# Performance work log

Measured on AMD Instinct MI355X. Metric: run time of the kernel, lower is better.

## Reference

```python
import jax, jax.numpy as jnp
import numpy as np

# Assumptions from DCalhas/eeg_to_fmri repo layers:
#  - RandomFourierFeatures: z = cos(x @ W + b) followed by layer normalization
#    over the feature axis (normalization='layer'), W/b trainable.
#  - Sinusoids: elementwise sin(x).

B, D, T, L = 64, 512, 1024, 512

def _layer_norm(x, eps=1e-5):
    mu = jnp.mean(x, axis=-1, keepdims=True)
    var = jnp.var(x, axis=-1, keepdims=True)
    return (x - mu) * jax.lax.rsqrt(var + eps)

def setup_inputs() -> dict:
    key = jax.random.key(0)
    ks = jax.random.split(key, 12)
    s = 1.0 / np.sqrt(L)
    return {
        "x": jax.random.normal(ks[0], (B, D, T), jnp.float32),
        "rff_w": jax.random.normal(ks[1], (D, L), jnp.float32) * (1.0 / np.sqrt(D)),
        "rff_b": jax.random.uniform(ks[2], (L,), jnp.float32, 0.0, 2.0 * np.pi),
        "weight_input": jax.random.normal(ks[3], (L, L), jnp.float32) * s,
        "weight_forget": jax.random.normal(ks[4], (L, L), jnp.float32) * s,
        "weight_context": jax.random.normal(ks[5], (L, L), jnp.float32) * s,
        "recurrent_input": jax.random.normal(ks[6], (L, L), jnp.float32) * s,
        "recurrent_forget": jax.random.normal(ks[7], (L, L), jnp.float32) * s,
        "recurrent_context": jax.random.normal(ks[8], (L, L), jnp.float32) * s,
        "bias_input": jnp.zeros((L,), jnp.float32),
        "bias_forget": jnp.zeros((L,), jnp.float32),
        "bias_context": jnp.zeros((L,), jnp.float32),
        "init_latent": jax.random.normal(ks[9], (1, 1, L), jnp.float32) * s,
        "init_context": jax.random.normal(ks[10], (1, 1, L), jnp.float32) * s,
    }

def reference(x, rff_w, rff_b, weight_input, weight_forget, weight_context,
              recurrent_input, recurrent_forget, recurrent_context,
              bias_input, bias_forget, bias_context, init_latent, init_context):
    b = x.shape[0]
    xt = jnp.transpose(x, (0, 2, 1))                      # [B,T,D]
    z = _layer_norm(jnp.cos(xt @ rff_w + rff_b))          # [B,T,L]
    # hidden_states[t+1] = z_t in the original loop, so the "recurrent" input
    # at step t is z_{t-1} (init_latent at t=0). Gates are thus batchable.
    z_prev = jnp.concatenate(
        [jnp.broadcast_to(init_latent, (b, 1, z.shape[2])), z[:, :-1]], axis=1)
    i = jax.nn.sigmoid(z @ weight_input + z_prev @ recurrent_input + bias_input)
    f = jax.nn.sigmoid(z @ weight_forget + z_prev @ recurrent_forget + bias_forget)
    g = jnp.tanh(z @ weight_context + z_prev @ recurrent_context + bias_context)
    o = jnp.sin(z)                                        # Sinusoids gate

    c0 = jnp.broadcast_to(init_context[:, 0], (b, z.shape[2]))  # [B,L]
    def step(c_prev, gates):
        i_t, f_t, g_t, o_t = gates
        c_t = f_t * c_prev + i_t * g_t
        return c_t, o_t * c_t
    xs = tuple(jnp.transpose(a, (1, 0, 2)) for a in (i, f, g, o))  # time-major
    _, h = jax.lax.scan(step, c0, xs)                     # [T,B,L]
    return jnp.transpose(h, (1, 2, 0))                    # [B,L,T]
```

## Files before the change

### kernel.cpp

```cpp
#include <hip/hip_runtime.h>
#include <hip/hip_bf16.h>
#include <hip/hip_fp16.h>
#include <cstdint>
#include <cstddef>


typedef float f32x4 __attribute__((ext_vector_type(4)));
typedef short s16x8 __attribute__((ext_vector_type(8)));

__device__ __forceinline__ void gload_lds16(const void* g, void* l) {
  __builtin_amdgcn_global_load_lds(
      (const __attribute__((address_space(1))) void*)g,
      (__attribute__((address_space(3))) void*)l, 16, 0, 0);
}
__device__ __forceinline__ ushort f2bf(float f) {
  uint32_t u = __float_as_uint(f);
  return (ushort)((u + 0x7FFF + ((u >> 16) & 1)) >> 16);
}
__device__ __forceinline__ float bf2f(ushort s) {
  return __uint_as_float(((uint32_t)s) << 16);
}
__device__ __forceinline__ ushort f2h(float f) {
  return __half_as_ushort(__float2half(f));
}
__device__ __forceinline__ float h2f(ushort s) {
  return __half2float(__ushort_as_half(s));
}

#define MF(d, a, b) d = __builtin_amdgcn_mfma_f32_16x16x32_bf16(a, b, d, 0, 0, 0);

__global__ __launch_bounds__(256) void transpose8(
    const float* __restrict__ s0, const float* __restrict__ s1,
    const float* __restrict__ s2, const float* __restrict__ s3,
    const float* __restrict__ s4, const float* __restrict__ s5,
    const float* __restrict__ il, const float* __restrict__ W1,
    ushort* __restrict__ W2t, ushort* __restrict__ ilb,
    ushort* __restrict__ W1t)
{
  const int z = blockIdx.z;
  if (z == 6) {
    if (blockIdx.x == 0 && blockIdx.y == 0) {
      ilb[threadIdx.x] = f2bf(il[threadIdx.x]);
      ilb[threadIdx.x + 256] = f2bf(il[threadIdx.x + 256]);
    }
    return;
  }
  const float* src = z == 0 ? s0 : z == 1 ? s1 : z == 2 ? s2
                   : z == 3 ? s3 : z == 4 ? s4 : z == 5 ? s5 : W1;
  ushort* dst = (z == 7) ? W1t
              : W2t + (size_t)(z >> 1) * 512 * 1024 + (z & 1) * 512;
  const int ld = (z == 7) ? 512 : 1024;
  __shared__ float tile[32][33];
  const int c0 = blockIdx.x * 32, r0 = blockIdx.y * 32;
  const int tx = threadIdx.x & 31, ty = threadIdx.x >> 5;
#pragma unroll
  for (int i = 0; i < 4; ++i)
    tile[ty + i * 8][tx] = src[(size_t)(r0 + ty + i * 8) * 512 + c0 + tx];
  __syncthreads();
#pragma unroll
  for (int i = 0; i < 4; ++i)
    dst[(size_t)(c0 + ty + i * 8) * ld + r0 + tx] = f2bf(tile[tx][ty + i * 8]);
}

__global__ __launch_bounds__(256) void transpose_x(
    const float* __restrict__ x, ushort* __restrict__ xt)
{
  __shared__ float tile[64][68];
  const int b = blockIdx.z;
  const int t0 = blockIdx.x * 64, d0 = blockIdx.y * 64;
  const float* src = x + ((size_t)b * 512 + d0) * 1024 + t0;
  const int lr_ = threadIdx.x >> 4, lc4 = (threadIdx.x & 15) * 4;
#pragma unroll
  for (int p = 0; p < 4; ++p) {
    const float4 v = *(const float4*)(src + (size_t)(lr_ + p * 16) * 1024 + lc4);
    *(float4*)&tile[lr_ + p * 16][lc4] = v;
  }
  __syncthreads();
  const int tt = threadIdx.x >> 2, dc = (threadIdx.x & 3) * 16;
  ushort* dst = xt + ((size_t)b * 1024 + t0 + tt) * 512 + d0 + dc;
  uint4 o1, o2;
  o1.x = (uint)f2bf(tile[dc + 0][tt]) | ((uint)f2bf(tile[dc + 1][tt]) << 16);
  o1.y = (uint)f2bf(tile[dc + 2][tt]) | ((uint)f2bf(tile[dc + 3][tt]) << 16);
  o1.z = (uint)f2bf(tile[dc + 4][tt]) | ((uint)f2bf(tile[dc + 5][tt]) << 16);
  o1.w = (uint)f2bf(tile[dc + 6][tt]) | ((uint)f2bf(tile[dc + 7][tt]) << 16);
  o2.x = (uint)f2bf(tile[dc + 8][tt]) | ((uint)f2bf(tile[dc + 9][tt]) << 16);
  o2.y = (uint)f2bf(tile[dc + 10][tt]) | ((uint)f2bf(tile[dc + 11][tt]) << 16);
  o2.z = (uint)f2bf(tile[dc + 12][tt]) | ((uint)f2bf(tile[dc + 13][tt]) << 16);
  o2.w = (uint)f2bf(tile[dc + 14][tt]) | ((uint)f2bf(tile[dc + 15][tt]) << 16);
  *(uint4*)(dst) = o1;
  *(uint4*)(dst + 8) = o2;
}

__global__ __launch_bounds__(256, 2) void k1_mfma(
    const ushort* __restrict__ A, const ushort* __restrict__ Bt,
    const float* __restrict__ bias, ushort* __restrict__ U)
{
  __shared__ __align__(16) short As[128 * 64];
  __shared__ __align__(16) short Bs[128 * 64];
  const int tid = threadIdx.x;
  const int lane = tid & 63, wid = tid >> 6;
  const int orig = blockIdx.x;
  const int swz = (orig & 7) * 256 + (orig >> 3);
  const int n0 = (swz & 3) * 128, r0 = (swz >> 2) * 128;
  const int wr = wid >> 1, wc = wid & 1;
  const int fr = lane & 15, fq = lane >> 4;
  const int lr = lane >> 3;
  const int swz_el = ((lane & 7) ^ lr) * 8;

  const int RA = r0 + wid * 32 + lr;
  const ushort* pa0 = A + (size_t)(RA)      * 512 + swz_el;
  const ushort* pa1 = A + (size_t)(RA + 8)  * 512 + swz_el;
  const ushort* pa2 = A + (size_t)(RA + 16) * 512 + swz_el;
  const ushort* pa3 = A + (size_t)(RA + 24) * 512 + swz_el;
  const int RB = n0 + wid * 32 + lr;
  const ushort* pb0 = Bt + (size_t)(RB)      * 512 + swz_el;
  const ushort* pb1 = Bt + (size_t)(RB + 8)  * 512 + swz_el;
  const ushort* pb2 = Bt + (size_t)(RB + 16) * 512 + swz_el;
  const ushort* pb3 = Bt + (size_t)(RB + 24) * 512 + swz_el;
  char* dA = (char*)As + wid * 4096;
  char* dB = (char*)Bs + wid * 4096;

  const int so0 = fr * 64 + ((fq)     ^ (fr & 7)) * 8;
  const int so1 = fr * 64 + ((4 + fq) ^ (fr & 7)) * 8;

  f32x4 c00 = {0.f,0.f,0.f,0.f}, c01 = c00, c02 = c00, c03 = c00,
        c10 = c00, c11 = c00, c12 = c00, c13 = c00,
        c20 = c00, c21 = c00, c22 = c00, c23 = c00,
        c30 = c00, c31 = c00, c32 = c00, c33 = c00;

  for (int k0 = 0; k0 < 512; k0 += 64) {
    gload_lds16(pa0 + k0, dA);        gload_lds16(pa1 + k0, dA + 1024);
    gload_lds16(pa2 + k0, dA + 2048); gload_lds16(pa3 + k0, dA + 3072);
    gload_lds16(pb0 + k0, dB);        gload_lds16(pb1 + k0, dB + 1024);
    gload_lds16(pb2 + k0, dB + 2048); gload_lds16(pb3 + k0, dB + 3072);
    __syncthreads();
    const s16x8 a00 = *(const s16x8*)&As[wr * 4096 + 0 * 1024 + so0];
    const s16x8 a01 = *(const s16x8*)&As[wr * 4096 + 0 * 1024 + so1];
    const s16x8 a10 = *(const s16x8*)&As[wr * 4096 + 1 * 1024 + so0];
    const s16x8 a11 = *(const s16x8*)&As[wr * 4096 + 1 * 1024 + so1];
    const s16x8 a20 = *(const s16x8*)&As[wr * 4096 + 2 * 1024 + so0];
    const s16x8 a21 = *(const s16x8*)&As[wr * 4096 + 2 * 1024 + so1];
    const s16x8 a30 = *(const s16x8*)&As[wr * 4096 + 3 * 1024 + so0];
    const s16x8 a31 = *(const s16x8*)&As[wr * 4096 + 3 * 1024 + so1];
    const s16x8 b00 = *(const s16x8*)&Bs[wc * 4096 + 0 * 1024 + so0];
    const s16x8 b01 = *(const s16x8*)&Bs[wc * 4096 + 0 * 1024 + so1];
    const s16x8 b10 = *(const s16x8*)&Bs[wc * 4096 + 1 * 1024 + so0];
    const s16x8 b11 = *(const s16x8*)&Bs[wc * 4096 + 1 * 1024 + so1];
    const s16x8 b20 = *(const s16x8*)&Bs[wc * 4096 + 2 * 1024 + so0];
    const s16x8 b21 = *(const s16x8*)&Bs[wc * 4096 + 2 * 1024 + so1];
    const s16x8 b30 = *(const s16x8*)&Bs[wc * 4096 + 3 * 1024 + so0];
    const s16x8 b31 = *(const s16x8*)&Bs[wc * 4096 + 3 * 1024 + so1];
    MF(c00, a00, b00) MF(c01, a00, b10) MF(c02, a00, b20) MF(c03, a00, b30)
    MF(c10, a10, b00) MF(c11, a10, b10) MF(c12, a10, b20) MF(c13, a10, b30)
    MF(c20, a20, b00) MF(c21, a20, b10) MF(c22, a20, b20) MF(c23, a20, b30)
    MF(c30, a30, b00) MF(c31, a30, b10) MF(c32, a30, b20) MF(c33, a30, b30)
    MF(c00, a01, b01) MF(c01, a01, b11) MF(c02, a01, b21) MF(c03, a01, b31)
    MF(c10, a11, b01) MF(c11, a11, b11) MF(c12, a11, b21) MF(c13, a11, b31)
    MF(c20, a21, b01) MF(c21, a21, b11) MF(c22, a21, b21) MF(c23, a21, b31)
    MF(c30, a31, b01) MF(c31, a31, b11) MF(c32, a31, b21) MF(c33, a31, b31)
    __syncthreads();
  }

#define EPI1(cmn, m_, n_) { \
    const int col = n0 + wc * 64 + n_ * 16 + fr; \
    const float bv = bias[col]; \
    const int rbase = r0 + wr * 64 + m_ * 16 + fq * 4; \
    _Pragma("unroll") for (int j = 0; j < 4; ++j) \
      U[(size_t)(rbase + j) * 512 + col] = f2bf(cosf(cmn[j] + bv)); }
  EPI1(c00, 0, 0) EPI1(c01, 0, 1) EPI1(c02, 0, 2) EPI1(c03, 0, 3)
  EPI1(c10, 1, 0) EPI1(c11, 1, 1) EPI1(c12, 1, 2) EPI1(c13, 1, 3)
  EPI1(c20, 2, 0) EPI1(c21, 2, 1) EPI1(c22, 2, 2) EPI1(c23, 2, 3)
  EPI1(c30, 3, 0) EPI1(c31, 3, 1) EPI1(c32, 3, 2) EPI1(c33, 3, 3)
#undef EPI1
}

__global__ __launch_bounds__(256) void ln_rows(
    const ushort* __restrict__ U, ushort* __restrict__ Z)
{
  const int row = blockIdx.x * 4 + (threadIdx.x >> 6);
  const int lane = threadIdx.x & 63;
  const size_t base = (size_t)row * 512 + lane * 8;
  const uint4 pk = *(const uint4*)(U + base);
  float v[8];
  v[0] = bf2f(pk.x & 0xffff); v[1] = bf2f(pk.x >> 16);
  v[2] = bf2f(pk.y & 0xffff); v[3] = bf2f(pk.y >> 16);
  v[4] = bf2f(pk.z & 0xffff); v[5] = bf2f(pk.z >> 16);
  v[6] = bf2f(pk.w & 0xffff); v[7] = bf2f(pk.w >> 16);
  float s = 0.f, s2 = 0.f;
#pragma unroll
  for (int j = 0; j < 8; ++j) { s += v[j]; s2 += v[j] * v[j]; }
#pragma unroll
  for (int m = 1; m < 64; m <<= 1) { s += __shfl_xor(s, m); s2 += __shfl_xor(s2, m); }
  const float mean = s * (1.f / 512.f);
  const float var = s2 * (1.f / 512.f) - mean * mean;
  const float inv = rsqrtf(var + 1e-5f);
  uint4 o;
  o.x = (uint)f2bf((v[0] - mean) * inv) | ((uint)f2bf((v[1] - mean) * inv) << 16);
  o.y = (uint)f2bf((v[2] - mean) * inv) | ((uint)f2bf((v[3] - mean) * inv) << 16);
  o.z = (uint)f2bf((v[4] - mean) * inv) | ((uint)f2bf((v[5] - mean) * inv) << 16);
  o.w = (uint)f2bf((v[6] - mean) * inv) | ((uint)f2bf((v[7] - mean) * inv) << 16);
  *(uint4*)(Z + base) = o;
}

__global__ __launch_bounds__(256, 2) void k2_mfma(
    const ushort* __restrict__ Z, const ushort* __restrict__ Wt,
    const ushort* __restrict__ IL,
    const float* __restrict__ biv, const float* __restrict__ bfv,
    const float* __restrict__ bcv,
    ushort* __restrict__ G2, int tc, int Tc, int nwg)
{
  __shared__ __align__(16) short As[128 * 64];
  __shared__ __align__(16) short Bs0[128 * 64];
  __shared__ __align__(16) short Bs1[128 * 64];
  const int tid = threadIdx.x;
  const int lane = tid & 63, wid = tid >> 6;
  const int cpx = nwg >> 3;
  const int orig = blockIdx.x;
  const int swz = (orig & 7) * cpx + (orig >> 3);
  const int bx = swz % 6, by = swz / 6;
  const int nb = Tc >> 7;
  const int b = by / nb, tb = by % nb;
  const int r0g = b * 1024 + tc + tb * 128;
  const int r0c = b * Tc + tb * 128;
  const bool isig = bx < 4;
  const int n0 = isig ? bx * 128 : 0;
  const int fb = bx - 4;
  const int wr = wid >> 1, wc = wid & 1;
  const int fr = lane & 15, fq = lane >> 4;
  const int lr = lane >> 3;
  const int swz_el = ((lane & 7) ^ lr) * 8;

  const int R0 = r0g + wid * 32 + lr;
  const ushort* pa0 = Z + (size_t)(R0)      * 512 + swz_el;
  const ushort* pa1 = Z + (size_t)(R0 + 8)  * 512 + swz_el;
  const ushort* pa2 = Z + (size_t)(R0 + 16) * 512 + swz_el;
  const ushort* pa3 = Z + (size_t)(R0 + 24) * 512 + swz_el;
  const ushort* ph0 = ((((R0)      & 1023) == 0) ? IL : (Z + (size_t)(R0 - 1)  * 512)) + swz_el;
  const ushort* ph1 = ((((R0 + 8)  & 1023) == 0) ? IL : (Z + (size_t)(R0 + 7)  * 512)) + swz_el;
  const ushort* ph2 = ((((R0 + 16) & 1023) == 0) ? IL : (Z + (size_t)(R0 + 15) * 512)) + swz_el;
  const ushort* ph3 = ((((R0 + 24) & 1023) == 0) ? IL : (Z + (size_t)(R0 + 23) * 512)) + swz_el;
  const int RB0 = (isig ? n0 : 512 + fb * 256) + wid * 32 + lr;
  const ushort* pb0 = Wt + (size_t)(RB0)      * 1024 + swz_el;
  const ushort* pb1 = Wt + (size_t)(RB0 + 8)  * 1024 + swz_el;
  const ushort* pb2 = Wt + (size_t)(RB0 + 16) * 1024 + swz_el;
  const ushort* pb3 = Wt + (size_t)(RB0 + 24) * 1024 + swz_el;
  const int RB1 = (isig ? 1024 + n0 : 512 + fb * 256 + 128) + wid * 32 + lr;
  const ushort* pq0 = Wt + (size_t)(RB1)      * 1024 + swz_el;
  const ushort* pq1 = Wt + (size_t)(RB1 + 8)  * 1024 + swz_el;
  const ushort* pq2 = Wt + (size_t)(RB1 + 16) * 1024 + swz_el;
  const ushort* pq3 = Wt + (size_t)(RB1 + 24) * 1024 + swz_el;

  const int so0 = fr * 64 + ((fq)     ^ (fr & 7)) * 8;
  const int so1 = fr * 64 + ((4 + fq) ^ (fr & 7)) * 8;

  f32x4 zz = {0.f,0.f,0.f,0.f};
  f32x4 c00=zz,c01=zz,c02=zz,c03=zz, c10=zz,c11=zz,c12=zz,c13=zz,
        c20=zz,c21=zz,c22=zz,c23=zz, c30=zz,c31=zz,c32=zz,c33=zz;
  f32x4 d00=zz,d01=zz,d02=zz,d03=zz, d10=zz,d11=zz,d12=zz,d13=zz,
        d20=zz,d21=zz,d22=zz,d23=zz, d30=zz,d31=zz,d32=zz,d33=zz;

#define STG8(P0,P1,P2,P3, KO, DST) { \
    char* d_ = (char*)(DST) + wid * 4096; \
    gload_lds16((P0) + (KO), d_);        gload_lds16((P1) + (KO), d_ + 1024); \
    gload_lds16((P2) + (KO), d_ + 2048); gload_lds16((P3) + (KO), d_ + 3072); }

#define RDA(SO) \
    const s16x8 fa0 = *(const s16x8*)&As[wr * 4096 + 0 * 1024 + (SO)]; \
    const s16x8 fa1 = *(const s16x8*)&As[wr * 4096 + 1 * 1024 + (SO)]; \
    const s16x8 fa2 = *(const s16x8*)&As[wr * 4096 + 2 * 1024 + (SO)]; \
    const s16x8 fa3 = *(const s16x8*)&As[wr * 4096 + 3 * 1024 + (SO)];

#define RDB(BS, SO) \
    const s16x8 fb0 = *(const s16x8*)&(BS)[wc * 4096 + 0 * 1024 + (SO)]; \
    const s16x8 fb1 = *(const s16x8*)&(BS)[wc * 4096 + 1 * 1024 + (SO)]; \
    const s16x8 fb2 = *(const s16x8*)&(BS)[wc * 4096 + 2 * 1024 + (SO)]; \
    const s16x8 fb3 = *(const s16x8*)&(BS)[wc * 4096 + 3 * 1024 + (SO)];

#define MMC \
    MF(c00,fa0,fb0) MF(c01,fa0,fb1) MF(c02,fa0,fb2) MF(c03,fa0,fb3) \
    MF(c10,fa1,fb0) MF(c11,fa1,fb1) MF(c12,fa1,fb2) MF(c13,fa1,fb3) \
    MF(c20,fa2,fb0) MF(c21,fa2,fb1) MF(c22,fa2,fb2) MF(c23,fa2,fb3) \
    MF(c30,fa3,fb0) MF(c31,fa3,fb1) MF(c32,fa3,fb2) MF(c33,fa3,fb3)

#define MMD \
    MF(d00,fa0,fb0) MF(d01,fa0,fb1) MF(d02,fa0,fb2) MF(d03,fa0,fb3) \
    MF(d10,fa1,fb0) MF(d11,fa1,fb1) MF(d12,fa1,fb2) MF(d13,fa1,fb3) \
    MF(d20,fa2,fb0) MF(d21,fa2,fb1) MF(d22,fa2,fb2) MF(d23,fa2,fb3) \
    MF(d30,fa3,fb0) MF(d31,fa3,fb1) MF(d32,fa3,fb2) MF(d33,fa3,fb3)

#define KSTEP(SO_) { \
    RDA(SO_) \
    { RDB(Bs0, SO_) MMC } \
    { RDB(Bs1, SO_) MMD } }

  for (int k0 = 0; k0 < 512; k0 += 64) {
    STG8(pa0, pa1, pa2, pa3, k0, As)
    STG8(pb0, pb1, pb2, pb3, k0, Bs0)
    STG8(pq0, pq1, pq2, pq3, k0, Bs1)
    __syncthreads();
    KSTEP(so0)
    KSTEP(so1)
    __syncthreads();
  }
  for (int k0 = 0; k0 < 512; k0 += 64) {
    STG8(ph0, ph1, ph2, ph3, k0, As)
    STG8(pb0, pb1, pb2, pb3, 512 + k0, Bs0)
    STG8(pq0, pq1, pq2, pq3, 512 + k0, Bs1)
    __syncthreads();
    KSTEP(so0)
    KSTEP(so1)
    __syncthreads();
  }
#undef KSTEP
#undef MMD
#undef MMC
#undef RDB
#undef RDA
#undef STG8

  if (isig) {
#define EPI(cmn, dmn, m_, n_) { \
    const int col = n0 + wc * 64 + n_ * 16 + fr; \
    const float bvi = biv[col], bvc = bcv[col]; \
    const int rbase = wr * 64 + m_ * 16 + fq * 4; \
    _Pragma("unroll") for (int j = 0; j < 4; ++j) { \
      const float iv = 1.f / (1.f + __expf(-(cmn[j] + bvi))); \
      const float gv = 2.f / (1.f + __expf(-2.f * (dmn[j] + bvc))) - 1.f; \
      G2[(size_t)(r0c + rbase + j) * 1024 + col] = f2h(iv * gv); } }
    EPI(c00, d00, 0, 0) EPI(c01, d01, 0, 1) EPI(c02, d02, 0, 2) EPI(c03, d03, 0, 3)
    EPI(c10, d10, 1, 0) EPI(c11, d11, 1, 1) EPI(c12, d12, 1, 2) EPI(c13, d13, 1, 3)
    EPI(c20, d20, 2, 0) EPI(c21, d21, 2, 1) EPI(c22, d22, 2, 2) EPI(c23, d23, 2, 3)
    EPI(c30, d30, 3, 0) EPI(c31, d31, 3, 1) EPI(c32, d32, 3, 2) EPI(c33, d33, 3, 3)
#undef EPI
  } else {
#define EPIF(cmn, m_, n_, COFF) { \
    const int col = fb * 256 + (COFF) + wc * 64 + n_ * 16 + fr; \
    const float bv = bfv[col]; \
    const int rbase = wr * 64 + m_ * 16 + fq * 4; \
    _Pragma("unroll") for (int j = 0; j < 4; ++j) { \
      const float fv = 1.f / (1.f + __expf(-(cmn[j] + bv))); \
      G2[(size_t)(r0c + rbase + j) * 1024 + 512 + col] = f2h(fv); } }
    EPIF(c00, 0, 0, 0) EPIF(c01, 0, 1, 0) EPIF(c02, 0, 2, 0) EPIF(c03, 0, 3, 0)
    EPIF(c10, 1, 0, 0) EPIF(c11, 1, 1, 0) EPIF(c12, 1, 2, 0) EPIF(c13, 1, 3, 0)
    EPIF(c20, 2, 0, 0) EPIF(c21, 2, 1, 0) EPIF(c22, 2, 2, 0) EPIF(c23, 2, 3, 0)
    EPIF(c30, 3, 0, 0) EPIF(c31, 3, 1, 0) EPIF(c32, 3, 2, 0) EPIF(c33, 3, 3, 0)
    EPIF(d00, 0, 0, 128) EPIF(d01, 0, 1, 128) EPIF(d02, 0, 2, 128) EPIF(d03, 0, 3, 128)
    EPIF(d10, 1, 0, 128) EPIF(d11, 1, 1, 128) EPIF(d12, 1, 2, 128) EPIF(d13, 1, 3, 128)
    EPIF(d20, 2, 0, 128) EPIF(d21, 2, 1, 128) EPIF(d22, 2, 2, 128) EPIF(d23, 2, 3, 128)
    EPIF(d30, 3, 0, 128) EPIF(d31, 3, 1, 128) EPIF(d32, 3, 2, 128) EPIF(d33, 3, 3, 128)
#undef EPIF
  }
}

__global__ __launch_bounds__(256) void k3a_seg(
    const ushort* __restrict__ G2, float* __restrict__ Aseg,
    float* __restrict__ Bseg, int Tc)
{
  const int l = blockIdx.x * 256 + threadIdx.x;
  const int b = blockIdx.y, s = blockIdx.z;
  const int SEGc = Tc >> 6;
  const ushort* gb = G2 + ((size_t)(b * Tc + s * 64)) * 1024 + l;
  float A = 1.f, c = 0.f;
#pragma unroll 8
  for (int j = 0; j < 64; ++j) {
    const float P = h2f(gb[(size_t)j * 1024]);
    const float F = h2f(gb[(size_t)j * 1024 + 512]);
    A *= F;
    c = fmaf(F, c, P);
  }
  const size_t o = (size_t)(b * SEGc + s) * 512 + l;
  Aseg[o] = A;
  Bseg[o] = c;
}

__global__ __launch_bounds__(512) void k3b_comb(
    const float* __restrict__ Aseg, const float* __restrict__ Bseg,
    const float* __restrict__ initc, float* __restrict__ cstart,
    float* __restrict__ cbuf, int tc, int Tc)
{
  const int b = blockIdx.x, l = threadIdx.x;
  const int SEGc = Tc >> 6;
  float c = (tc == 0) ? initc[l] : cbuf[b * 512 + l];
  for (int s = 0; s < SEGc; ++s) {
    const size_t o = (size_t)(b * SEGc + s) * 512 + l;
    cstart[o] = c;
    c = fmaf(Aseg[o], c, Bseg[o]);
  }
  cbuf[b * 512 + l] = c;
}

__global__ __launch_bounds__(128) void k3c_emit(
    const ushort* __restrict__ G2, const ushort* __restrict__ Z,
    const float* __restrict__ cstart, float* __restrict__ out,
    int tc, int Tc)
{
  __shared__ float tile[128][65];
  const int tid = threadIdx.x;
  const int l0 = blockIdx.x * 128;
  const int b = blockIdx.y, s = blockIdx.z;
  const int SEGc = Tc >> 6;
  const int l = l0 + tid;

  float c = cstart[(size_t)(b * SEGc + s) * 512 + l];
  const ushort* gb = G2 + ((size_t)(b * Tc + s * 64)) * 1024 + l;
  const ushort* zb = Z + ((size_t)(b * 1024 + tc + s * 64)) * 512 + l;
#pragma unroll 8
  for (int j = 0; j < 64; ++j) {
    const float P = h2f(gb[(size_t)j * 1024]);
    const float F = h2f(gb[(size_t)j * 1024 + 512]);
    const float zv = bf2f(zb[(size_t)j * 512]);
    c = fmaf(F, c, P);
    tile[tid][j] = sinf(zv) * c;
  }
  __syncthreads();
  const int col = tid & 63, rhalf = tid >> 6;
  const size_t obase = ((size_t)b * 512 + l0) * 1024 + (size_t)(tc + s * 64) + col;
#pragma unroll
  for (int p = 0; p < 64; ++p) {
    const int row = rhalf + p * 2;
    out[obase + (size_t)row * 1024] = tile[row][col];
  }
}

extern "C" void kernel_launch(void* const* d_in, const int* in_sizes, int n_in,
                              void* d_out, int out_size, void* d_ws, size_t ws_size,
                              hipStream_t stream)
{
  const float* x  = (const float*)d_in[0];
  const float* W  = (const float*)d_in[1];
  const float* rb = (const float*)d_in[2];
  const float* wi = (const float*)d_in[3];
  const float* wf = (const float*)d_in[4];
  const float* wc = (const float*)d_in[5];
  const float* ri = (const float*)d_in[6];
  const float* rf = (const float*)d_in[7];
  const float* rc = (const float*)d_in[8];
  const float* bi = (const float*)d_in[9];
  const float* bfo = (const float*)d_in[10];
  const float* bc = (const float*)d_in[11];
  const float* il = (const float*)d_in[12];
  const float* ic = (const float*)d_in[13];
  float* out = (float*)d_out;

  char* ws = (char*)d_ws;
  size_t off = 0;
  auto alloc = [&](size_t bytes) -> void* {
    void* p = ws + off;
    off = (off + bytes + 255) & ~(size_t)255;
    return p;
  };
  ushort* z    = (ushort*)alloc((size_t)65536 * 512 * 2);
  ushort* W1t  = (ushort*)alloc((size_t)512 * 512 * 2);
  ushort* W2t  = (ushort*)alloc((size_t)1536 * 1024 * 2);
  ushort* ilb  = (ushort*)alloc(512 * 2);
  float*  cbuf = (float*)alloc((size_t)64 * 512 * 4);
  float*  Aseg = (float*)alloc((size_t)64 * 16 * 512 * 4);
  float*  Bseg = (float*)alloc((size_t)64 * 16 * 512 * 4);
  float*  cstart = (float*)alloc((size_t)64 * 16 * 512 * 4);
  const size_t fixed_end = off;
  ushort* xt   = (ushort*)alloc((size_t)65536 * 512 * 2);
  ushort* G2   = (ushort*)(ws + fixed_end);
  ushort* u    = (ushort*)d_out;

  int Tc = 1024;
  while (Tc > 128 && fixed_end + (size_t)64 * Tc * 1024 * 2 > ws_size) Tc >>= 1;

  transpose8<<<dim3(16, 16, 8), 256, 0, stream>>>(
      wi, ri, wf, rf, wc, rc, il, W, W2t, ilb, W1t);
  transpose_x<<<dim3(16, 8, 64), 256, 0, stream>>>(x, xt);

  k1_mfma<<<dim3(2048), 256, 0, stream>>>(xt, W1t, rb, u);
  ln_rows<<<16384, 256, 0, stream>>>(u, z);

  for (int tc = 0; tc < 1024; tc += Tc) {
    const int SEGc = Tc >> 6;
    const int nwg2 = 6 * 64 * (Tc >> 7);
    k2_mfma<<<dim3(nwg2), 256, 0, stream>>>(
        z, W2t, ilb, bi, bfo, bc, G2, tc, Tc, nwg2);
    k3a_seg<<<dim3(2, 64, SEGc), 256, 0, stream>>>(G2, Aseg, Bseg, Tc);
    k3b_comb<<<64, 512, 0, stream>>>(Aseg, Bseg, ic, cstart, cbuf, tc, Tc);
    k3c_emit<<<dim3(4, 64, SEGc), 128, 0, stream>>>(G2, z, cstart, out, tc, Tc);
  }
}
```

Before: 534.9 us.

## Fuse layer norm into RFF GEMM epilogue with full-row 64x512 tiles

The first GEMM now computes whole 64-row by 512-column output tiles per block, so cos and the layer-norm statistics can be computed in the epilogue using shuffle and shared-memory reductions. The normalized bf16 result is written directly to z. This removes the separate ln_rows kernel and the bf16 round trip through an intermediate buffer. In exchange LDS use grows (the whole 512x64 B slice is staged each k-step), there are 32 accumulator tiles per wave, and the grid is halved, which may cut occupancy.

After: 636.6 us. 19.0% more time.

```diff
diff --git a/kernel.cpp b/kernel.cpp
--- a/kernel.cpp
+++ b/kernel.cpp
@@ -93,113 +93,127 @@
 
 __global__ __launch_bounds__(256, 2) void k1_mfma(
     const ushort* __restrict__ A, const ushort* __restrict__ Bt,
-    const float* __restrict__ bias, ushort* __restrict__ U)
-{
-  __shared__ __align__(16) short As[128 * 64];
-  __shared__ __align__(16) short Bs[128 * 64];
+    const float* __restrict__ bias, ushort* __restrict__ Z)
+{
+  __shared__ __align__(16) short As[64 * 64];
+  __shared__ __align__(16) short Bs[512 * 64];
+  __shared__ float redS[4][64], redS2[4][64], redM[64], redI[64];
   const int tid = threadIdx.x;
   const int lane = tid & 63, wid = tid >> 6;
   const int orig = blockIdx.x;
-  const int swz = (orig & 7) * 256 + (orig >> 3);
-  const int n0 = (swz & 3) * 128, r0 = (swz >> 2) * 128;
-  const int wr = wid >> 1, wc = wid & 1;
+  const int swz = (orig & 7) * 128 + (orig >> 3);
+  const int r0 = swz * 64;
   const int fr = lane & 15, fq = lane >> 4;
   const int lr = lane >> 3;
   const int swz_el = ((lane & 7) ^ lr) * 8;
 
-  const int RA = r0 + wid * 32 + lr;
-  const ushort* pa0 = A + (size_t)(RA)      * 512 + swz_el;
-  const ushort* pa1 = A + (size_t)(RA + 8)  * 512 + swz_el;
-  const ushort* pa2 = A + (size_t)(RA + 16) * 512 + swz_el;
-  const ushort* pa3 = A + (size_t)(RA + 24) * 512 + swz_el;
-  const int RB = n0 + wid * 32 + lr;
-  const ushort* pb0 = Bt + (size_t)(RB)      * 512 + swz_el;
-  const ushort* pb1 = Bt + (size_t)(RB + 8)  * 512 + swz_el;
-  const ushort* pb2 = Bt + (size_t)(RB + 16) * 512 + swz_el;
-  const ushort* pb3 = Bt + (size_t)(RB + 24) * 512 + swz_el;
-  char* dA = (char*)As + wid * 4096;
-  char* dB = (char*)Bs + wid * 4096;
-
-  const int so0 = fr * 64 + ((fq)     ^ (fr & 7)) * 8;
-  const int so1 = fr * 64 + ((4 + fq) ^ (fr & 7)) * 8;
-
-  f32x4 c00 = {0.f,0.f,0.f,0.f}, c01 = c00, c02 = c00, c03 = c00,
-        c10 = c00, c11 = c00, c12 = c00, c13 = c00,
-        c20 = c00, c21 = c00, c22 = c00, c23 = c00,
-        c30 = c00, c31 = c00, c32 = c00, c33 = c00;
+  const int RA = r0 + wid * 16 + lr;
+  const ushort* pa0 = A + (size_t)(RA)     * 512 + swz_el;
+  const ushort* pa1 = A + (size_t)(RA + 8) * 512 + swz_el;
+  const ushort* pb = Bt + (size_t)(wid * 128 + lr) * 512 + swz_el;
+  char* dA = (char*)As + wid * 2048;
+  char* dB = (char*)Bs + wid * 16384;
+
+  const int so0 = ((fq)     ^ (fr & 7)) * 8;
+  const int so1 = ((4 + fq) ^ (fr & 7)) * 8;
+
+  f32x4 zz = {0.f,0.f,0.f,0.f};
+  f32x4 c00=zz,c01=zz,c02=zz,c03=zz,c04=zz,c05=zz,c06=zz,c07=zz,
+        c10=zz,c11=zz,c12=zz,c13=zz,c14=zz,c15=zz,c16=zz,c17=zz,
+        c20=zz,c21=zz,c22=zz,c23=zz,c24=zz,c25=zz,c26=zz,c27=zz,
+        c30=zz,c31=zz,c32=zz,c33=zz,c34=zz,c35=zz,c36=zz,c37=zz;
+
+#define KS(SO_) { \
+    const s16x8 fa0 = *(const s16x8*)&As[(0 * 16 + fr) * 64 + (SO_)]; \
+    const s16x8 fa1 = *(const s16x8*)&As[(1 * 16 + fr) * 64 + (SO_)]; \
+    const s16x8 fa2 = *(const s16x8*)&As[(2 * 16 + fr) * 64 + (SO_)]; \
+    const s16x8 fa3 = *(const s16x8*)&As[(3 * 16 + fr) * 64 + (SO_)]; \
+    const s16x8 fb0 = *(const s16x8*)&Bs[(wid * 128 + 0 * 16 + fr) * 64 + (SO_)]; \
+    const s16x8 fb1 = *(const s16x8*)&Bs[(wid * 128 + 1 * 16 + fr) * 64 + (SO_)]; \
+    const s16x8 fb2 = *(const s16x8*)&Bs[(wid * 128 + 2 * 16 + fr) * 64 + (SO_)]; \
+    const s16x8 fb3 = *(const s16x8*)&Bs[(wid * 128 + 3 * 16 + fr) * 64 + (SO_)]; \
+    const s16x8 fb4 = *(const s16x8*)&Bs[(wid * 128 + 4 * 16 + fr) * 64 + (SO_)]; \
+    const s16x8 fb5 = *(const s16x8*)&Bs[(wid * 128 + 5 * 16 + fr) * 64 + (SO_)]; \
+    const s16x8 fb6 = *(const s16x8*)&Bs[(wid * 128 + 6 * 16 + fr) * 64 + (SO_)]; \
+    const s16x8 fb7 = *(const s16x8*)&Bs[(wid * 128 + 7 * 16 + fr) * 64 + (SO_)]; \
+    MF(c00,fa0,fb0) MF(c01,fa0,fb1) MF(c02,fa0,fb2) MF(c03,fa0,fb3) \
+    MF(c04,fa0,fb4) MF(c05,fa0,fb5) MF(c06,fa0,fb6) MF(c07,fa0,fb7) \
+    MF(c10,fa1,fb0) MF(c11,fa1,fb1) MF(c12,fa1,fb2) MF(c13,fa1,fb3) \
+    MF(c14,fa1,fb4) MF(c15,fa1,fb5) MF(c16,fa1,fb6) MF(c17,fa1,fb7) \
+    MF(c20,fa2,fb0) MF(c21,fa2,fb1) MF(c22,fa2,fb2) MF(c23,fa2,fb3) \
+    MF(c24,fa2,fb4) MF(c25,fa2,fb5) MF(c26,fa2,fb6) MF(c27,fa2,fb7) \
+    MF(c30,fa3,fb0) MF(c31,fa3,fb1) MF(c32,fa3,fb2) MF(c33,fa3,fb3) \
+    MF(c34,fa3,fb4) MF(c35,fa3,fb5) MF(c36,fa3,fb6) MF(c37,fa3,fb7) }
 
   for (int k0 = 0; k0 < 512; k0 += 64) {
-    gload_lds16(pa0 + k0, dA);        gload_lds16(pa1 + k0, dA + 1024);
-    gload_lds16(pa2 + k0, dA + 2048); gload_lds16(pa3 + k0, dA + 3072);
-    gload_lds16(pb0 + k0, dB);        gload_lds16(pb1 + k0, dB + 1024);
-    gload_lds16(pb2 + k0, dB + 2048); gload_lds16(pb3 + k0, dB + 3072);
-    __syncthreads();
-    const s16x8 a00 = *(const s16x8*)&As[wr * 4096 + 0 * 1024 + so0];
-    const s16x8 a01 = *(const s16x8*)&As[wr * 4096 + 0 * 1024 + so1];
-    const s16x8 a10 = *(const s16x8*)&As[wr * 4096 + 1 * 1024 + so0];
-    const s16x8 a11 = *(const s16x8*)&As[wr * 4096 + 1 * 1024 + so1];
-    const s16x8 a20 = *(const s16x8*)&As[wr * 4096 + 2 * 1024 + so0];
-    const s16x8 a21 = *(const s16x8*)&As[wr * 4096 + 2 * 1024 + so1];
-    const s16x8 a30 = *(const s16x8*)&As[wr * 4096 + 3 * 1024 + so0];
-    const s16x8 a31 = *(const s16x8*)&As[wr * 4096 + 3 * 1024 + so1];
-    const s16x8 b00 = *(const s16x8*)&Bs[wc * 4096 + 0 * 1024 + so0];
-    const s16x8 b01 = *(const s16x8*)&Bs[wc * 4096 + 0 * 1024 + so1];
-    const s16x8 b10 = *(const s16x8*)&Bs[wc * 4096 + 1 * 1024 + so0];
-    const s16x8 b11 = *(const s16x8*)&Bs[wc * 4096 + 1 * 1024 + so1];
-    const s16x8 b20 = *(const s16x8*)&Bs[wc * 4096 + 2 * 1024 + so0];
-    const s16x8 b21 = *(const s16x8*)&Bs[wc * 4096 + 2 * 1024 + so1];
-    const s16x8 b30 = *(const s16x8*)&Bs[wc * 4096 + 3 * 1024 + so0];
-    const s16x8 b31 = *(const s16x8*)&Bs[wc * 4096 + 3 * 1024 + so1];
-    MF(c00, a00, b00) MF(c01, a00, b10) MF(c02, a00, b20) MF(c03, a00, b30)
-    MF(c10, a10, b00) MF(c11, a10, b10) MF(c12, a10, b20) MF(c13, a10, b30)
-    MF(c20, a20, b00) MF(c21, a20, b10) MF(c22, a20, b20) MF(c23, a20, b30)
-    MF(c30, a30, b00) MF(c31, a30, b10) MF(c32, a30, b20) MF(c33, a30, b30)
-    MF(c00, a01, b01) MF(c01, a01, b11) MF(c02, a01, b21) MF(c03, a01, b31)
-    MF(c10, a11, b01) MF(c11, a11, b11) MF(c12, a11, b21) MF(c13, a11, b31)
-    MF(c20, a21, b01) MF(c21, a21, b11) MF(c22, a21, b21) MF(c23, a21, b31)
-    MF(c30, a31, b01) MF(c31, a31, b11) MF(c32, a31, b21) MF(c33, a31, b31)
-    __syncthreads();
-  }
-
-#define EPI1(cmn, m_, n_) { \
-    const int col = n0 + wc * 64 + n_ * 16 + fr; \
-    const float bv = bias[col]; \
-    const int rbase = r0 + wr * 64 + m_ * 16 + fq * 4; \
-    _Pragma("unroll") for (int j = 0; j < 4; ++j) \
-      U[(size_t)(rbase + j) * 512 + col] = f2bf(cosf(cmn[j] + bv)); }
-  EPI1(c00, 0, 0) EPI1(c01, 0, 1) EPI1(c02, 0, 2) EPI1(c03, 0, 3)
-  EPI1(c10, 1, 0) EPI1(c11, 1, 1) EPI1(c12, 1, 2) EPI1(c13, 1, 3)
-  EPI1(c20, 2, 0) EPI1(c21, 2, 1) EPI1(c22, 2, 2) EPI1(c23, 2, 3)
-  EPI1(c30, 3, 0) EPI1(c31, 3, 1) EPI1(c32, 3, 2) EPI1(c33, 3, 3)
-#undef EPI1
-}
-
-__global__ __launch_bounds__(256) void ln_rows(
-    const ushort* __restrict__ U, ushort* __restrict__ Z)
-{
-  const int row = blockIdx.x * 4 + (threadIdx.x >> 6);
-  const int lane = threadIdx.x & 63;
-  const size_t base = (size_t)row * 512 + lane * 8;
-  const uint4 pk = *(const uint4*)(U + base);
-  float v[8];
-  v[0] = bf2f(pk.x & 0xffff); v[1] = bf2f(pk.x >> 16);
-  v[2] = bf2f(pk.y & 0xffff); v[3] = bf2f(pk.y >> 16);
-  v[4] = bf2f(pk.z & 0xffff); v[5] = bf2f(pk.z >> 16);
-  v[6] = bf2f(pk.w & 0xffff); v[7] = bf2f(pk.w >> 16);
-  float s = 0.f, s2 = 0.f;
+    gload_lds16(pa0 + k0, dA);
+    gload_lds16(pa1 + k0, dA + 1024);
 #pragma unroll
-  for (int j = 0; j < 8; ++j) { s += v[j]; s2 += v[j] * v[j]; }
-#pragma unroll
-  for (int m = 1; m < 64; m <<= 1) { s += __shfl_xor(s, m); s2 += __shfl_xor(s2, m); }
-  const float mean = s * (1.f / 512.f);
-  const float var = s2 * (1.f / 512.f) - mean * mean;
-  const float inv = rsqrtf(var + 1e-5f);
-  uint4 o;
-  o.x = (uint)f2bf((v[0] - mean) * inv) | ((uint)f2bf((v[1] - mean) * inv) << 16);
-  o.y = (uint)f2bf((v[2] - mean) * inv) | ((uint)f2bf((v[3] - mean) * inv) << 16);
-  o.z = (uint)f2bf((v[4] - mean) * inv) | ((uint)f2bf((v[5] - mean) * inv) << 16);
-  o.w = (uint)f2bf((v[6] - mean) * inv) | ((uint)f2bf((v[7] - mean) * inv) << 16);
-  *(uint4*)(Z + base) = o;
+    for (int g = 0; g < 16; ++g)
+      gload_lds16(pb + (size_t)g * 8 * 512 + k0, dB + g * 1024);
+    __syncthreads();
+    KS(so0)
+    KS(so1)
+    __syncthreads();
+  }
+#undef KS
+
+  f32x4 ps0 = zz, ps1 = zz, ps2 = zz, ps3 = zz;
+  f32x4 pq0 = zz, pq1 = zz, pq2 = zz, pq3 = zz;
+#define CB(d, mm, n_) { \
+    const float bv = bias[wid * 128 + n_ * 16 + fr]; \
+    f32x4 t; \
+    _Pragma("unroll") for (int j = 0; j < 4; ++j) t[j] = cosf(d[j] + bv); \
+    d = t; ps##mm += t; pq##mm += t * t; }
+  CB(c00,0,0) CB(c01,0,1) CB(c02,0,2) CB(c03,0,3)
+  CB(c04,0,4) CB(c05,0,5) CB(c06,0,6) CB(c07,0,7)
+  CB(c10,1,0) CB(c11,1,1) CB(c12,1,2) CB(c13,1,3)
+  CB(c14,1,4) CB(c15,1,5) CB(c16,1,6) CB(c17,1,7)
+  CB(c20,2,0) CB(c21,2,1) CB(c22,2,2) CB(c23,2,3)
+  CB(c24,2,4) CB(c25,2,5) CB(c26,2,6) CB(c27,2,7)
+  CB(c30,3,0) CB(c31,3,1) CB(c32,3,2) CB(c33,3,3)
+  CB(c34,3,4) CB(c35,3,5) CB(c36,3,6) CB(c37,3,7)
+#undef CB
+
+#define RED2(PS, PQ, m_) \
+  _Pragma("unroll") for (int j = 0; j < 4; ++j) { \
+    float s = PS[j], s2 = PQ[j]; \
+    _Pragma("unroll") for (int msk = 1; msk < 16; msk <<= 1) { \
+      s += __shfl_xor(s, msk); s2 += __shfl_xor(s2, msk); } \
+    if (fr == 0) { \
+      redS[wid][m_ * 16 + fq * 4 + j] = s; \
+      redS2[wid][m_ * 16 + fq * 4 + j] = s2; } }
+  RED2(ps0, pq0, 0)
+  RED2(ps1, pq1, 1)
+  RED2(ps2, pq2, 2)
+  RED2(ps3, pq3, 3)
+#undef RED2
+  __syncthreads();
+  if (tid < 64) {
+    const float s  = redS[0][tid] + redS[1][tid] + redS[2][tid] + redS[3][tid];
+    const float s2 = redS2[0][tid] + redS2[1][tid] + redS2[2][tid] + redS2[3][tid];
+    const float mean = s * (1.f / 512.f);
+    const float var = s2 * (1.f / 512.f) - mean * mean;
+    redM[tid] = mean;
+    redI[tid] = rsqrtf(var + 1e-5f);
+  }
+  __syncthreads();
+
+  ushort* Zp = Z + (size_t)r0 * 512;
+#define ZW(d, m_, n_) { \
+    _Pragma("unroll") for (int j = 0; j < 4; ++j) { \
+      const int row = m_ * 16 + fq * 4 + j; \
+      Zp[(size_t)row * 512 + wid * 128 + n_ * 16 + fr] = \
+          f2bf((d[j] - redM[row]) * redI[row]); } }
+  ZW(c00,0,0) ZW(c01,0,1) ZW(c02,0,2) ZW(c03,0,3)
+  ZW(c04,0,4) ZW(c05,0,5) ZW(c06,0,6) ZW(c07,0,7)
+  ZW(c10,1,0) ZW(c11,1,1) ZW(c12,1,2) ZW(c13,1,3)
+  ZW(c14,1,4) ZW(c15,1,5) ZW(c16,1,6) ZW(c17,1,7)
+  ZW(c20,2,0) ZW(c21,2,1) ZW(c22,2,2) ZW(c23,2,3)
+  ZW(c24,2,4) ZW(c25,2,5) ZW(c26,2,6) ZW(c27,2,7)
+  ZW(c30,3,0) ZW(c31,3,1) ZW(c32,3,2) ZW(c33,3,3)
+  ZW(c34,3,4) ZW(c35,3,5) ZW(c36,3,6) ZW(c37,3,7)
+#undef ZW
 }
 
 __global__ __launch_bounds__(256, 2) void k2_mfma(
@@ -460,7 +474,6 @@
   const size_t fixed_end = off;
   ushort* xt   = (ushort*)alloc((size_t)65536 * 512 * 2);
   ushort* G2   = (ushort*)(ws + fixed_end);
-  ushort* u    = (ushort*)d_out;
 
   int Tc = 1024;
   while (Tc > 128 && fixed_end + (size_t)64 * Tc * 1024 * 2 > ws_size) Tc >>= 1;
@@ -469,8 +482,7 @@
       wi, ri, wf, rf, wc, rc, il, W, W2t, ilb, W1t);
   transpose_x<<<dim3(16, 8, 64), 256, 0, stream>>>(x, xt);
 
-  k1_mfma<<<dim3(2048), 256, 0, stream>>>(xt, W1t, rb, u);
-  ln_rows<<<16384, 256, 0, stream>>>(u, z);
+  k1_mfma<<<dim3(1024), 256, 0, stream>>>(xt, W1t, rb, z);
 
   for (int tc = 0; tc < 1024; tc += Tc) {
     const int SEGc = Tc >> 6;
```

## Merge prep transposes and fold segment combine into emit kernel

Applied to the files above, without the earlier changes.

Combines the weight transpose and x transpose into one launch, removes the serial k3b combine kernel by having each emit block recompute its segment start carry from the per-segment A/B values, and vectorises the segment scan to two lanes per thread with packed loads. The goal is fewer kernel launches and dropping the cstart buffer round-trip. In exchange there is redundant prefix work in every emit block, and the prep launch now includes many early-exit blocks. The recompute loop is hardcoded to 15 segments and stays correct only while SEGc is at most 16.

New measurement: 532.9 us. Within noise of the previous version (-0.4%).

```diff
diff --git a/kernel.cpp b/kernel.cpp
--- a/kernel.cpp
+++ b/kernel.cpp
@@ -29,15 +29,44 @@
 
 #define MF(d, a, b) d = __builtin_amdgcn_mfma_f32_16x16x32_bf16(a, b, d, 0, 0, 0);
 
-__global__ __launch_bounds__(256) void transpose8(
+__global__ __launch_bounds__(256) void prep_all(
     const float* __restrict__ s0, const float* __restrict__ s1,
     const float* __restrict__ s2, const float* __restrict__ s3,
     const float* __restrict__ s4, const float* __restrict__ s5,
     const float* __restrict__ il, const float* __restrict__ W1,
+    const float* __restrict__ x,
     ushort* __restrict__ W2t, ushort* __restrict__ ilb,
-    ushort* __restrict__ W1t)
-{
+    ushort* __restrict__ W1t, ushort* __restrict__ xt)
+{
+  __shared__ float tile[64][68];
   const int z = blockIdx.z;
+  if (z >= 8) {
+    if (blockIdx.y >= 8) return;
+    const int b = z - 8;
+    const int t0 = blockIdx.x * 64, d0 = blockIdx.y * 64;
+    const float* src = x + ((size_t)b * 512 + d0) * 1024 + t0;
+    const int lr_ = threadIdx.x >> 4, lc4 = (threadIdx.x & 15) * 4;
+#pragma unroll
+    for (int p = 0; p < 4; ++p) {
+      const float4 v = *(const float4*)(src + (size_t)(lr_ + p * 16) * 1024 + lc4);
+      *(float4*)&tile[lr_ + p * 16][lc4] = v;
+    }
+    __syncthreads();
+    const int tt = threadIdx.x >> 2, dc = (threadIdx.x & 3) * 16;
+    ushort* dst = xt + ((size_t)b * 1024 + t0 + tt) * 512 + d0 + dc;
+    uint4 o1, o2;
+    o1.x = (uint)f2bf(tile[dc + 0][tt]) | ((uint)f2bf(tile[dc + 1][tt]) << 16);
+    o1.y = (uint)f2bf(tile[dc + 2][tt]) | ((uint)f2bf(tile[dc + 3][tt]) << 16);
+    o1.z = (uint)f2bf(tile[dc + 4][tt]) | ((uint)f2bf(tile[dc + 5][tt]) << 16);
+    o1.w = (uint)f2bf(tile[dc + 6][tt]) | ((uint)f2bf(tile[dc + 7][tt]) << 16);
+    o2.x = (uint)f2bf(tile[dc + 8][tt]) | ((uint)f2bf(tile[dc + 9][tt]) << 16);
+    o2.y = (uint)f2bf(tile[dc + 10][tt]) | ((uint)f2bf(tile[dc + 11][tt]) << 16);
+    o2.z = (uint)f2bf(tile[dc + 12][tt]) | ((uint)f2bf(tile[dc + 13][tt]) << 16);
+    o2.w = (uint)f2bf(tile[dc + 14][tt]) | ((uint)f2bf(tile[dc + 15][tt]) << 16);
+    *(uint4*)(dst) = o1;
+    *(uint4*)(dst + 8) = o2;
+    return;
+  }
   if (z == 6) {
     if (blockIdx.x == 0 && blockIdx.y == 0) {
       ilb[threadIdx.x] = f2bf(il[threadIdx.x]);
@@ -50,45 +79,16 @@
   ushort* dst = (z == 7) ? W1t
               : W2t + (size_t)(z >> 1) * 512 * 1024 + (z & 1) * 512;
   const int ld = (z == 7) ? 512 : 1024;
-  __shared__ float tile[32][33];
+  float (*t32)[33] = (float(*)[33])&tile[0][0];
   const int c0 = blockIdx.x * 32, r0 = blockIdx.y * 32;
   const int tx = threadIdx.x & 31, ty = threadIdx.x >> 5;
 #pragma unroll
   for (int i = 0; i < 4; ++i)
-    tile[ty + i * 8][tx] = src[(size_t)(r0 + ty + i * 8) * 512 + c0 + tx];
+    t32[ty + i * 8][tx] = src[(size_t)(r0 + ty + i * 8) * 512 + c0 + tx];
   __syncthreads();
 #pragma unroll
   for (int i = 0; i < 4; ++i)
-    dst[(size_t)(c0 + ty + i * 8) * ld + r0 + tx] = f2bf(tile[tx][ty + i * 8]);
-}
-
-__global__ __launch_bounds__(256) void transpose_x(
-    const float* __restrict__ x, ushort* __restrict__ xt)
-{
-  __shared__ float tile[64][68];
-  const int b = blockIdx.z;
-  const int t0 = blockIdx.x * 64, d0 = blockIdx.y * 64;
-  const float* src = x + ((size_t)b * 512 + d0) * 1024 + t0;
-  const int lr_ = threadIdx.x >> 4, lc4 = (threadIdx.x & 15) * 4;
-#pragma unroll
-  for (int p = 0; p < 4; ++p) {
-    const float4 v = *(const float4*)(src + (size_t)(lr_ + p * 16) * 1024 + lc4);
-    *(float4*)&tile[lr_ + p * 16][lc4] = v;
-  }
-  __syncthreads();
-  const int tt = threadIdx.x >> 2, dc = (threadIdx.x & 3) * 16;
-  ushort* dst = xt + ((size_t)b * 1024 + t0 + tt) * 512 + d0 + dc;
-  uint4 o1, o2;
-  o1.x = (uint)f2bf(tile[dc + 0][tt]) | ((uint)f2bf(tile[dc + 1][tt]) << 16);
-  o1.y = (uint)f2bf(tile[dc + 2][tt]) | ((uint)f2bf(tile[dc + 3][tt]) << 16);
-  o1.z = (uint)f2bf(tile[dc + 4][tt]) | ((uint)f2bf(tile[dc + 5][tt]) << 16);
-  o1.w = (uint)f2bf(tile[dc + 6][tt]) | ((uint)f2bf(tile[dc + 7][tt]) << 16);
-  o2.x = (uint)f2bf(tile[dc + 8][tt]) | ((uint)f2bf(tile[dc + 9][tt]) << 16);
-  o2.y = (uint)f2bf(tile[dc + 10][tt]) | ((uint)f2bf(tile[dc + 11][tt]) << 16);
-  o2.z = (uint)f2bf(tile[dc + 12][tt]) | ((uint)f2bf(tile[dc + 13][tt]) << 16);
-  o2.w = (uint)f2bf(tile[dc + 14][tt]) | ((uint)f2bf(tile[dc + 15][tt]) << 16);
-  *(uint4*)(dst) = o1;
-  *(uint4*)(dst + 8) = o2;
+    dst[(size_t)(c0 + ty + i * 8) * ld + r0 + tx] = f2bf(t32[tx][ty + i * 8]);
 }
 
 __global__ __launch_bounds__(256, 2) void k1_mfma(
@@ -356,43 +356,32 @@
     const ushort* __restrict__ G2, float* __restrict__ Aseg,
     float* __restrict__ Bseg, int Tc)
 {
-  const int l = blockIdx.x * 256 + threadIdx.x;
-  const int b = blockIdx.y, s = blockIdx.z;
+  const int l2 = threadIdx.x * 2;
+  const int b = blockIdx.x, s = blockIdx.y;
   const int SEGc = Tc >> 6;
-  const ushort* gb = G2 + ((size_t)(b * Tc + s * 64)) * 1024 + l;
-  float A = 1.f, c = 0.f;
+  const ushort* gb = G2 + ((size_t)(b * Tc + s * 64)) * 1024;
+  float A0 = 1.f, A1 = 1.f, c0 = 0.f, c1 = 0.f;
 #pragma unroll 8
   for (int j = 0; j < 64; ++j) {
-    const float P = h2f(gb[(size_t)j * 1024]);
-    const float F = h2f(gb[(size_t)j * 1024 + 512]);
-    A *= F;
-    c = fmaf(F, c, P);
-  }
-  const size_t o = (size_t)(b * SEGc + s) * 512 + l;
-  Aseg[o] = A;
-  Bseg[o] = c;
-}
-
-__global__ __launch_bounds__(512) void k3b_comb(
-    const float* __restrict__ Aseg, const float* __restrict__ Bseg,
-    const float* __restrict__ initc, float* __restrict__ cstart,
-    float* __restrict__ cbuf, int tc, int Tc)
-{
-  const int b = blockIdx.x, l = threadIdx.x;
-  const int SEGc = Tc >> 6;
-  float c = (tc == 0) ? initc[l] : cbuf[b * 512 + l];
-  for (int s = 0; s < SEGc; ++s) {
-    const size_t o = (size_t)(b * SEGc + s) * 512 + l;
-    cstart[o] = c;
-    c = fmaf(Aseg[o], c, Bseg[o]);
-  }
-  cbuf[b * 512 + l] = c;
+    const uint Pp = *(const uint*)(gb + (size_t)j * 1024 + l2);
+    const uint Fp = *(const uint*)(gb + (size_t)j * 1024 + 512 + l2);
+    const float P0 = h2f((ushort)(Pp & 0xffff)), P1 = h2f((ushort)(Pp >> 16));
+    const float F0 = h2f((ushort)(Fp & 0xffff)), F1 = h2f((ushort)(Fp >> 16));
+    A0 *= F0; A1 *= F1;
+    c0 = fmaf(F0, c0, P0); c1 = fmaf(F1, c1, P1);
+  }
+  const size_t o = (size_t)(b * SEGc + s) * 512 + l2;
+  float2 av; av.x = A0; av.y = A1;
+  float2 bv; bv.x = c0; bv.y = c1;
+  *(float2*)(Aseg + o) = av;
+  *(float2*)(Bseg + o) = bv;
 }
 
 __global__ __launch_bounds__(128) void k3c_emit(
     const ushort* __restrict__ G2, const ushort* __restrict__ Z,
-    const float* __restrict__ cstart, float* __restrict__ out,
-    int tc, int Tc)
+    const float* __restrict__ Aseg, const float* __restrict__ Bseg,
+    const float* __restrict__ initc, float* __restrict__ cbuf,
+    float* __restrict__ out, int tc, int Tc)
 {
   __shared__ float tile[128][65];
   const int tid = threadIdx.x;
@@ -401,7 +390,14 @@
   const int SEGc = Tc >> 6;
   const int l = l0 + tid;
 
-  float c = cstart[(size_t)(b * SEGc + s) * 512 + l];
+  float c = (tc == 0) ? initc[l] : cbuf[b * 512 + l];
+#pragma unroll
+  for (int sp = 0; sp < 15; ++sp) {
+    const size_t o = (size_t)(b * SEGc + sp) * 512 + l;
+    const float Av = Aseg[o], Bv = Bseg[o];
+    c = (sp < s) ? fmaf(Av, c, Bv) : c;
+  }
+
   const ushort* gb = G2 + ((size_t)(b * Tc + s * 64)) * 1024 + l;
   const ushort* zb = Z + ((size_t)(b * 1024 + tc + s * 64)) * 512 + l;
 #pragma unroll 8
@@ -412,6 +408,7 @@
     c = fmaf(F, c, P);
     tile[tid][j] = sinf(zv) * c;
   }
+  if (s == SEGc - 1) cbuf[b * 512 + l] = c;
   __syncthreads();
   const int col = tid & 63, rhalf = tid >> 6;
   const size_t obase = ((size_t)b * 512 + l0) * 1024 + (size_t)(tc + s * 64) + col;
@@ -456,7 +453,6 @@
   float*  cbuf = (float*)alloc((size_t)64 * 512 * 4);
   float*  Aseg = (float*)alloc((size_t)64 * 16 * 512 * 4);
   float*  Bseg = (float*)alloc((size_t)64 * 16 * 512 * 4);
-  float*  cstart = (float*)alloc((size_t)64 * 16 * 512 * 4);
   const size_t fixed_end = off;
   ushort* xt   = (ushort*)alloc((size_t)65536 * 512 * 2);
   ushort* G2   = (ushort*)(ws + fixed_end);
@@ -465,9 +461,8 @@
   int Tc = 1024;
   while (Tc > 128 && fixed_end + (size_t)64 * Tc * 1024 * 2 > ws_size) Tc >>= 1;
 
-  transpose8<<<dim3(16, 16, 8), 256, 0, stream>>>(
-      wi, ri, wf, rf, wc, rc, il, W, W2t, ilb, W1t);
-  transpose_x<<<dim3(16, 8, 64), 256, 0, stream>>>(x, xt);
+  prep_all<<<dim3(16, 16, 72), 256, 0, stream>>>(
+      wi, ri, wf, rf, wc, rc, il, W, x, W2t, ilb, W1t, xt);
 
   k1_mfma<<<dim3(2048), 256, 0, stream>>>(xt, W1t, rb, u);
   ln_rows<<<16384, 256, 0, stream>>>(u, z);
@@ -477,8 +472,8 @@
     const int nwg2 = 6 * 64 * (Tc >> 7);
     k2_mfma<<<dim3(nwg2), 256, 0, stream>>>(
         z, W2t, ilb, bi, bfo, bc, G2, tc, Tc, nwg2);
-    k3a_seg<<<dim3(2, 64, SEGc), 256, 0, stream>>>(G2, Aseg, Bseg, Tc);
-    k3b_comb<<<64, 512, 0, stream>>>(Aseg, Bseg, ic, cstart, cbuf, tc, Tc);
-    k3c_emit<<<dim3(4, 64, SEGc), 128, 0, stream>>>(G2, z, cstart, out, tc, Tc);
-  }
-}
+    k3a_seg<<<dim3(64, SEGc), 256, 0, stream>>>(G2, Aseg, Bseg, Tc);
+    k3c_emit<<<dim3(4, 64, SEGc), 128, 0, stream>>>(
+        G2, z, Aseg, Bseg, ic, cbuf, out, tc, Tc);
+  }
+}
```
